# Kernel tuning notes

Hardware: AMD Instinct MI355X
Metric: run time of the kernel (lower is better)

## Reference

```python
import jax, jax.numpy as jnp
import numpy as np

V, E, H, B, P, Q = 100000, 300, 256, 64, 400, 50
NEG = -1e7


def _gru_param(k, s=0.08):
    k1, k2, k3, k4 = jax.random.split(k, 4)
    return (jax.random.normal(k1, (2, 3 * H, E)) * s,
            jax.random.normal(k2, (2, 3 * H, H)) * s,
            jax.random.normal(k3, (2, 3 * H)) * s,
            jax.random.normal(k4, (2, 3 * H)) * s)


def setup_inputs() -> dict:
    key = jax.random.key(0)
    ks = jax.random.split(key, 10)
    emb = (jax.random.normal(ks[0], (V, E)) * 0.1).at[0].set(0.0)  # padding_idx=0 row zeroed
    passage = jax.random.randint(ks[1], (B, P), 1, V)
    question = jax.random.randint(ks[2], (B, Q), 1, V)
    # variable lengths, padding (token 0) at the tail like pack_padded_sequence assumes
    p_len = 200 + (jnp.arange(B) * 7) % (P - 200)
    q_len = 20 + (jnp.arange(B) * 3) % (Q - 20)
    passage = jnp.where(jnp.arange(P)[None, :] < p_len[:, None], passage, 0)
    question = jnp.where(jnp.arange(Q)[None, :] < q_len[:, None], question, 0)
    pW_ih, pW_hh, pb_ih, pb_hh = _gru_param(ks[3])
    qW_ih, qW_hh, qb_ih, qb_hh = _gru_param(ks[4])
    start_w = jax.random.normal(ks[5], (6 * H,)) * 0.05
    start_b = jax.random.normal(ks[6], ()) * 0.05
    end_w = jax.random.normal(ks[7], (6 * H,)) * 0.05
    end_b = jax.random.normal(ks[8], ()) * 0.05
    return dict(passage=passage, question=question, emb=emb,
                pW_ih=pW_ih, pW_hh=pW_hh, pb_ih=pb_ih, pb_hh=pb_hh,
                qW_ih=qW_ih, qW_hh=qW_hh, qb_ih=qb_ih, qb_hh=qb_hh,
                start_w=start_w, start_b=start_b, end_w=end_w, end_b=end_b)


def bi_gru(x, mask, Wih, Whh, bih, bhh):
    """Bidirectional GRU with packed-sequence-equivalent masking.
    x: (B,T,E), mask: (B,T) float. Returns (B,T,2H). Padded outputs are 0,
    and the backward pass starts at the true last token (mask freezes state)."""
    m = mask[..., None]                                          # (B,T,1)
    xproj = jnp.einsum('bte,dhe->dbth', x, Wih) + bih[:, None, None, :]  # (2,B,T,3H)

    def run(xp, mm, Whh_d, bhh_d):
        def step(h, inp):
            xt, mt = inp                                         # (B,3H),(B,1)
            hp = h @ Whh_d.T + bhh_d
            r = jax.nn.sigmoid(xt[:, :H] + hp[:, :H])
            z = jax.nn.sigmoid(xt[:, H:2 * H] + hp[:, H:2 * H])
            n = jnp.tanh(xt[:, 2 * H:] + r * hp[:, 2 * H:])
            h_new = (1 - z) * n + z * h
            h_new = mt * h_new + (1 - mt) * h
            return h_new, h_new * mt
        h0 = jnp.zeros((xp.shape[0], H), xp.dtype)
        _, out = jax.lax.scan(step, h0, (xp.transpose(1, 0, 2), mm.transpose(1, 0, 2)))
        return out.transpose(1, 0, 2)                            # (B,T,H)

    fwd = run(xproj[0], m, Whh[0], bhh[0])
    bwd = run(xproj[1][:, ::-1], m[:, ::-1], Whh[1], bhh[1])[:, ::-1]
    return jnp.concatenate([fwd, bwd], axis=-1)


def reference(passage, question, emb,
              pW_ih, pW_hh, pb_ih, pb_hh,
              qW_ih, qW_hh, qb_ih, qb_hh,
              start_w, start_b, end_w, end_b):
    p_mask = (passage != 0).astype(jnp.float32)                  # (B,P)
    q_mask = (question != 0).astype(jnp.float32)                 # (B,Q)
    Hp = bi_gru(emb[passage], p_mask, pW_ih, pW_hh, pb_ih, pb_hh)  # (B,P,2H)
    Hq = bi_gru(emb[question], q_mask, qW_ih, qW_hh, qb_ih, qb_hh)  # (B,Q,2H)

    # Trilinear attention: decompose Linear over the cat([p, q, p*q]) terms
    w1, w2, w3 = start_w[:2 * H], start_w[2 * H:4 * H], start_w[4 * H:]
    scores = (Hp @ w1)[:, :, None] + (Hq @ w2)[:, None, :] \
        + jnp.einsum('bpd,bqd->bpq', Hp * w3, Hq) + start_b      # (B,P,Q)

    # allennlp masked_softmax: softmax(vector*mask) * mask, renormalized
    a = jax.nn.softmax(scores * q_mask[:, None, :], axis=-1) * q_mask[:, None, :]
    a = a / (a.sum(axis=-1, keepdims=True) + 1e-13)

    wavg = jnp.einsum('bpq,bqd->bpd', a, Hq)                     # (B,P,2H)
    combined = jnp.concatenate([Hp, wavg, Hp * wavg], axis=-1)   # (B,P,6H)

    start_logits = jnp.where(p_mask > 0, combined @ start_w + start_b, NEG)
    end_logits = jnp.where(p_mask > 0, combined @ end_w + end_b, NEG)
    log_mask = jnp.log(p_mask + 1e-45)
    softmax_start = jax.nn.log_softmax(start_logits + log_mask, axis=-1)
    softmax_end = jax.nn.log_softmax(end_logits + log_mask, axis=-1)
    return start_logits, end_logits, softmax_start, softmax_end
```

## Files before the change

kernel.cpp:

```cpp
#include <hip/hip_runtime.h>
#include <math.h>

constexpr int Bb = 64;
constexpr int Pp = 400;
constexpr int Qq = 50;
constexpr int Ee = 300;
constexpr int Hh = 256;
constexpr int H3 = 768;
constexpr int Dd = 512;

#define NEGC (-10000000.0f)
#define LOGTINY (-103.278929903f)

typedef _Float16 h2 __attribute__((ext_vector_type(2)));
typedef _Float16 f16x8 __attribute__((ext_vector_type(8)));
typedef float f32x4 __attribute__((ext_vector_type(4)));

__device__ __forceinline__ float allred(float v){
  #pragma unroll
  for (int off = 1; off < 64; off <<= 1) v += __shfl_xor(v, off);
  return v;
}
__device__ __forceinline__ float allmax(float v){
  #pragma unroll
  for (int off = 1; off < 64; off <<= 1) v = fmaxf(v, __shfl_xor(v, off));
  return v;
}
__device__ __forceinline__ float sigm(float x){ return 1.f / (1.f + expf(-x)); }

__device__ __forceinline__ float dot2f(unsigned a, unsigned b, float c){
#if __has_builtin(__builtin_amdgcn_fdot2)
  return __builtin_amdgcn_fdot2(__builtin_bit_cast(h2, a), __builtin_bit_cast(h2, b), c, false);
#else
  float r = c;
  asm("v_dot2_f32_f16 %0, %1, %2, %0" : "+v"(r) : "v"(a), "v"(b));
  return r;
#endif
}

#define U4C(v,c) ((c)==0?(v).x:((c)==1?(v).y:((c)==2?(v).z:(v).w)))

__global__ __launch_bounds__(256) void prep_emb16(const float* __restrict__ emb,
                                                  _Float16* __restrict__ emb16){
  size_t idx = (size_t)blockIdx.x * 256 + threadIdx.x;
  if (idx >= (size_t)100000 * 160) return;
  int col2 = (int)(idx % 160);
  size_t row = idx / 160;
  int c = col2 * 2;
  float2 v = make_float2(0.f, 0.f);
  if (c < Ee) v = *(const float2*)(emb + row * Ee + c);
  h2 o = { (_Float16)v.x, (_Float16)v.y };
  *(h2*)(emb16 + row * 320 + c) = o;
}

__global__ __launch_bounds__(256) void prep_wih16(const float* __restrict__ pW,
                                                  const float* __restrict__ qW,
                                                  _Float16* __restrict__ wih16){
  int idx = blockIdx.x * 256 + threadIdx.x;
  if (idx >= 2 * 2 * 768 * 160) return;
  int col2 = idx % 160;
  int r = idx / 160;
  int g = r / 1536;
  int dh = r % 1536;
  int c = col2 * 2;
  const float* W = g ? qW : pW;
  float2 v = make_float2(0.f, 0.f);
  if (c < Ee) v = *(const float2*)(W + (size_t)dh * Ee + c);
  h2 o = { (_Float16)v.x, (_Float16)v.y };
  *(h2*)(wih16 + (size_t)r * 320 + c) = o;
}

__global__ __launch_bounds__(256) void prep_w16(const float* __restrict__ pW,
                                                const float* __restrict__ qW,
                                                unsigned* __restrict__ w16){
  int idx = blockIdx.x * 256 + threadIdx.x;
  if (idx >= 2 * 2 * 3 * 16 * 512 * 4) return;
  int c = idx & 3;
  int t = (idx >> 2) & 511;
  int q = (idx >> 11) & 15;
  int gg = idx >> 15;
  int gate = gg % 3, gd = gg / 3;
  int d = gd & 1, g = gd >> 1;
  int j = t & 255, half = t >> 8;
  int p = half * 64 + q * 4 + c;
  int row = gate * 256 + j;
  const float* W = g ? qW : pW;
  const float* src = W + ((size_t)d * H3 + row) * Hh + 2 * p;
  _Float16 a = (_Float16)src[0], b = (_Float16)src[1];
  unsigned short ua, ub;
  __builtin_memcpy(&ua, &a, 2); __builtin_memcpy(&ub, &b, 2);
  unsigned val = (unsigned)ua | ((unsigned)ub << 16);

  size_t u4idx;
  if (q < 4)       u4idx = ((size_t)gg * 4 + q) * 512 + t;
  else if (q < 10) u4idx = 24576 + ((size_t)gg * 6 + (q - 4)) * 512 + t;
  else             u4idx = 61440 + ((size_t)gg * 6 + (q - 10)) * 512 + t;
  w16[u4idx * 4 + c] = val;
}

__global__ __launch_bounds__(512) void xproj_mfma(const int* __restrict__ tok,
                                                  const _Float16* __restrict__ emb16,
                                                  const _Float16* __restrict__ wih16,
                                                  const float* __restrict__ bih,
                                                  _Float16* __restrict__ xp, int T){
  __shared__ __align__(16) _Float16 Af[128][72];
  __shared__ __align__(16) _Float16 Bf[128][72];
  int tid = threadIdx.x;
  int m0 = blockIdx.y * 128;
  int nt = blockIdx.x;
  int d = nt / 6, h0 = (nt % 6) * 128;
  int wid = tid >> 6, lane = tid & 63;
  int wr = wid >> 2, wc = wid & 3;

  int r0 = tid >> 3;
  int r1 = (tid + 512) >> 3;
  int cc = (tid & 7) * 8;
  const _Float16* eA0 = emb16 + (size_t)tok[m0 + r0] * 320;
  const _Float16* eA1 = emb16 + (size_t)tok[m0 + r1] * 320;
  const _Float16* wB0 = wih16 + ((size_t)d * H3 + h0 + r0) * 320;
  const _Float16* wB1 = wih16 + ((size_t)d * H3 + h0 + r1) * 320;

  f32x4 acc[4][2] = {};

  for (int k0 = 0; k0 < 320; k0 += 64){
    *(f16x8*)&Af[r0][cc] = *(const f16x8*)(eA0 + k0 + cc);
    *(f16x8*)&Af[r1][cc] = *(const f16x8*)(eA1 + k0 + cc);
    *(f16x8*)&Bf[r0][cc] = *(const f16x8*)(wB0 + k0 + cc);
    *(f16x8*)&Bf[r1][cc] = *(const f16x8*)(wB1 + k0 + cc);
    __syncthreads();
    #pragma unroll
    for (int kc = 0; kc < 2; ++kc){
      int kb = kc * 32 + (lane >> 4) * 8;
      f16x8 af[4], bf[2];
      #pragma unroll
      for (int i = 0; i < 4; ++i) af[i] = *(const f16x8*)&Af[wr * 64 + i * 16 + (lane & 15)][kb];
      #pragma unroll
      for (int jn = 0; jn < 2; ++jn) bf[jn] = *(const f16x8*)&Bf[wc * 32 + jn * 16 + (lane & 15)][kb];
      #pragma unroll
      for (int i = 0; i < 4; ++i)
        #pragma unroll
        for (int jn = 0; jn < 2; ++jn)
          acc[i][jn] = __builtin_amdgcn_mfma_f32_16x16x32_f16(af[i], bf[jn], acc[i][jn], 0, 0, 0);
    }
    __syncthreads();
  }

  #pragma unroll
  for (int jn = 0; jn < 2; ++jn){
    int h = h0 + wc * 32 + jn * 16 + (lane & 15);
    float bv = bih[d * H3 + h];
    #pragma unroll
    for (int i = 0; i < 4; ++i){
      #pragma unroll
      for (int r = 0; r < 4; ++r){
        int m = m0 + wr * 64 + i * 16 + (lane >> 4) * 4 + r;
        int bI = m / T, tI = m - bI * T;
        xp[(((size_t)d * Bb + bI) * T + tI) * H3 + h] = (_Float16)(acc[i][jn][r] + bv);
      }
    }
  }
}

__global__ __launch_bounds__(512)
void gru_kernel(const int* __restrict__ ptok,
                const int* __restrict__ qtok,
                const _Float16* __restrict__ xpp,
                const _Float16* __restrict__ xpq,
                const unsigned* __restrict__ w16,
                const float* __restrict__ pbhh,
                const float* __restrict__ qbhh,
                float* __restrict__ Hp,
                float* __restrict__ Hq){
  int wg = blockIdx.x;
  bool isp = wg < 128;
  int lw = isp ? wg : wg - 128;
  int d = lw & 1, b = lw >> 1;
  int T = isp ? Pp : Qq;
  const int* tok = (isp ? ptok : qtok) + b * T;
  const _Float16* xrow = (isp ? xpp : xpq) + ((size_t)d * Bb + b) * T * H3;
  int gd = (isp ? 0 : 2) + d;
  const float* bhh = (isp ? pbhh : qbhh) + d * H3;
  float* Hout = (isp ? Hp : Hq) + (size_t)b * T * Dd + d * Hh;

  __shared__ __align__(16) uint4 ldsW[18 * 512];
  __shared__ unsigned hbuf[2][128];
  __shared__ float pa[Hh], pb[Hh], pn[Hh];

  int t = threadIdx.x;
  int j = t & 255, half = t >> 8, lane = t & 63;

  const uint4* wR = (const uint4*)w16 + (size_t)(gd * 3) * 4 * 512;
  unsigned wr0[16], wr1[16], wr2[16];
  #pragma unroll
  for (int q = 0; q < 4; ++q){
    uint4 v0 = wR[(0 * 4 + q) * 512 + t];
    uint4 v1 = wR[(1 * 4 + q) * 512 + t];
    uint4 v2 = wR[(2 * 4 + q) * 512 + t];
    wr0[4 * q + 0] = v0.x; wr0[4 * q + 1] = v0.y; wr0[4 * q + 2] = v0.z; wr0[4 * q + 3] = v0.w;
    wr1[4 * q + 0] = v1.x; wr1[4 * q + 1] = v1.y; wr1[4 * q + 2] = v1.z; wr1[4 * q + 3] = v1.w;
    wr2[4 * q + 0] = v2.x; wr2[4 * q + 1] = v2.y; wr2[4 * q + 2] = v2.z; wr2[4 * q + 3] = v2.w;
  }
  #pragma unroll
  for (int i = 0; i < 16; ++i){
    asm volatile("" : "+v"(wr0[i]));
    asm volatile("" : "+v"(wr1[i]));
    asm volatile("" : "+v"(wr2[i]));
  }
  const uint4* wL = (const uint4*)w16 + 24576 + (size_t)(gd * 3) * 6 * 512;
  #pragma unroll
  for (int u = 0; u < 18; ++u) ldsW[u * 512 + t] = wL[u * 512 + t];
  const uint4* wS = (const uint4*)w16 + 61440 + (size_t)(gd * 3) * 6 * 512;

  float bh0 = bhh[j], bh1 = bhh[Hh + j], bh2 = bhh[2 * Hh + j];
  float h_old = 0.f;
  if (t < 128) hbuf[1][t] = 0u;
  __syncthreads();

  int t0 = d ? (T - 1) : 0;
  float pre0 = 0.f, pre1 = 0.f, pre2 = 0.f;
  if (half == 0){
    pre0 = (float)xrow[(size_t)t0 * H3 + j];
    pre1 = (float)xrow[(size_t)t0 * H3 + Hh + j];
    pre2 = (float)xrow[(size_t)t0 * H3 + 2 * Hh + j];
  }

  for (int s = 0; s < T; ++s){
    int tt = d ? (T - 1 - s) : s;
    unsigned vh = hbuf[(s + 1) & 1][half * 64 + lane];
    float a0 = 0.f, a1 = 0.f, a2 = 0.f;

    uint4 sA0 = wS[0 * 512 + t], sA1 = wS[1 * 512 + t], sA2 = wS[2 * 512 + t],
          sA3 = wS[3 * 512 + t], sA4 = wS[4 * 512 + t], sA5 = wS[5 * 512 + t];
    uint4 sB0 = wS[6 * 512 + t],  sB1 = wS[7 * 512 + t],  sB2 = wS[8 * 512 + t],
          sB3 = wS[9 * 512 + t],  sB4 = wS[10 * 512 + t], sB5 = wS[11 * 512 + t];

    #pragma unroll
    for (int q = 0; q < 4; ++q)
      #pragma unroll
      for (int c = 0; c < 4; ++c){
        unsigned hv = (unsigned)__builtin_amdgcn_readlane((int)vh, q * 4 + c);
        a0 = dot2f(wr0[4 * q + c], hv, a0);
        a1 = dot2f(wr1[4 * q + c], hv, a1);
        a2 = dot2f(wr2[4 * q + c], hv, a2);
      }

    uint4 sC0 = wS[12 * 512 + t], sC1 = wS[13 * 512 + t], sC2 = wS[14 * 512 + t],
          sC3 = wS[15 * 512 + t], sC4 = wS[16 * 512 + t], sC5 = wS[17 * 512 + t];

    #pragma unroll
    for (int qb = 0; qb < 6; ++qb){
      uint4 l0 = ldsW[(0 * 6 + qb) * 512 + t];
      uint4 l1 = ldsW[(1 * 6 + qb) * 512 + t];
      uint4 l2 = ldsW[(2 * 6 + qb) * 512 + t];
      #pragma unroll
      for (int c = 0; c < 4; ++c){
        unsigned hv = (unsigned)__builtin_amdgcn_readlane((int)vh, 16 + qb * 4 + c);
        a0 = dot2f(U4C(l0, c), hv, a0);
        a1 = dot2f(U4C(l1, c), hv, a1);
        a2 = dot2f(U4C(l2, c), hv, a2);
      }
    }

    #define CONS(v, qi, ACC) { _Pragma("unroll") \
      for (int c = 0; c < 4; ++c){ \
        unsigned hv = (unsigned)__builtin_amdgcn_readlane((int)vh, 40 + (qi) * 4 + c); \
        ACC = dot2f(U4C(v, c), hv, ACC); } }
    CONS(sA0, 0, a0) CONS(sA1, 1, a0) CONS(sA2, 2, a0)
    CONS(sA3, 3, a0) CONS(sA4, 4, a0) CONS(sA5, 5, a0)
    CONS(sB0, 0, a1) CONS(sB1, 1, a1) CONS(sB2, 2, a1)
    CONS(sB3, 3, a1) CONS(sB4, 4, a1) CONS(sB5, 5, a1)
    CONS(sC0, 0, a2) CONS(sC1, 1, a2) CONS(sC2, 2, a2)
    CONS(sC3, 3, a2) CONS(sC4, 4, a2) CONS(sC5, 5, a2)
    #undef CONS

    if (half == 1){ pa[j] = a0; pb[j] = a1; pn[j] = a2; }
    __syncthreads();
    if (half == 0){
      float xt0 = pre0, xt1 = pre1, xt2 = pre2;
      if (s + 1 < T){
        int tn = d ? (T - 2 - s) : (s + 1);
        pre0 = (float)xrow[(size_t)tn * H3 + j];
        pre1 = (float)xrow[(size_t)tn * H3 + Hh + j];
        pre2 = (float)xrow[(size_t)tn * H3 + 2 * Hh + j];
      }
      float g0 = a0 + pa[j] + bh0;
      float g1 = a1 + pb[j] + bh1;
      float g2 = a2 + pn[j] + bh2;
      float r = sigm(xt0 + g0);
      float z = sigm(xt1 + g1);
      float n = tanhf(xt2 + r * g2);
      float hnew = (1.f - z) * n + z * h_old;
      float m = (tok[tt] != 0) ? 1.f : 0.f;
      float hm = m * hnew + (1.f - m) * h_old;
      h_old = hm;
      ((_Float16*)hbuf[s & 1])[j] = (_Float16)hm;
      Hout[(size_t)tt * Dd + j] = hm * m;
    }
    __syncthreads();
  }
}

__global__ __launch_bounds__(512) void attn_kernel(const float* __restrict__ Hp,
                                                   const float* __restrict__ Hq,
                                                   const int* __restrict__ ptok,
                                                   const int* __restrict__ qtok,
                                                   const float* __restrict__ start_w,
                                                   const float* __restrict__ sbp,
                                                   const float* __restrict__ end_w,
                                                   const float* __restrict__ ebp,
                                                   float* __restrict__ out){
  extern __shared__ __align__(16) float lds[];
  float* hqs = lds;
  float* s2s = hqs + Qq * Dd;
  float* qms = s2s + 64;
  float* scw = qms + 64;
  float* aw  = scw + 512;

  int b = blockIdx.y, pc = blockIdx.x;
  int tid = threadIdx.x, wid = tid >> 6, lane = tid & 63;
  float sb = sbp[0], eb = ebp[0];

  float w1r[8], w2r[8], w3r[8], e1r[8], e2r[8], e3r[8];
  #pragma unroll
  for (int i = 0; i < 8; ++i){
    int c = lane * 8 + i;
    w1r[i] = start_w[c]; w2r[i] = start_w[Dd + c]; w3r[i] = start_w[2 * Dd + c];
    e1r[i] = end_w[c];   e2r[i] = end_w[Dd + c];   e3r[i] = end_w[2 * Dd + c];
  }
  for (int idx = tid; idx < Qq * Dd; idx += 512) hqs[idx] = Hq[(size_t)b * Qq * Dd + idx];
  __syncthreads();

  for (int q = wid; q < Qq; q += 8){
    float part = 0.f;
    const float* hq = hqs + q * Dd + lane * 8;
    #pragma unroll
    for (int i = 0; i < 8; ++i) part += hq[i] * w2r[i];
    part = allred(part);
    if (lane == 0){
      s2s[q] = part;
      qms[q] = (qtok[b * Qq + q] != 0) ? 1.f : 0.f;
    }
  }
  __syncthreads();

  for (int p = pc * 100 + wid; p < pc * 100 + 100; p += 8){
    const float* hprow = Hp + ((size_t)b * Pp + p) * Dd + lane * 8;
    float4 hv0 = *(const float4*)hprow;
    float4 hv1 = *(const float4*)(hprow + 4);
    float hpc[8] = {hv0.x, hv0.y, hv0.z, hv0.w, hv1.x, hv1.y, hv1.z, hv1.w};
    float hw3[8], he3[8];
    float s1 = 0.f, ed = 0.f;
    #pragma unroll
    for (int i = 0; i < 8; ++i){
      hw3[i] = hpc[i] * w3r[i];
      he3[i] = hpc[i] * e3r[i];
      s1 += hpc[i] * w1r[i];
      ed += hpc[i] * e1r[i];
    }
    #pragma unroll
    for (int off = 1; off < 64; off <<= 1){
      s1 += __shfl_xor(s1, off);
      ed += __shfl_xor(ed, off);
    }
    for (int q = 0; q < Qq; ++q){
      const float4* hq4 = (const float4*)(hqs + q * Dd + lane * 8);
      float4 a0 = hq4[0], a1 = hq4[1];
      float dot = hw3[0] * a0.x + hw3[1] * a0.y + hw3[2] * a0.z + hw3[3] * a0.w
                + hw3[4] * a1.x + hw3[5] * a1.y + hw3[6] * a1.z + hw3[7] * a1.w;
      dot = allred(dot);
      if (lane == 0) scw[wid * 64 + q] = (s1 + s2s[q] + dot + sb) * qms[q];
    }
    float v = (lane < Qq) ? scw[wid * 64 + lane] : -1e30f;
    float M = allmax(v);
    float ev = (lane < Qq) ? expf(v - M) : 0.f;
    float S = allred(ev);
    float am = (lane < Qq) ? (ev / S) * qms[lane] : 0.f;
    float Sm = allred(am);
    float af = am / (Sm + 1e-13f);
    if (lane < Qq) aw[wid * 64 + lane] = af;
    float wv[8] = {0.f, 0.f, 0.f, 0.f, 0.f, 0.f, 0.f, 0.f};
    for (int q = 0; q < Qq; ++q){
      float aq = aw[wid * 64 + q];
      const float4* hq4 = (const float4*)(hqs + q * Dd + lane * 8);
      float4 a0 = hq4[0], a1 = hq4[1];
      wv[0] += aq * a0.x; wv[1] += aq * a0.y; wv[2] += aq * a0.z; wv[3] += aq * a0.w;
      wv[4] += aq * a1.x; wv[5] += aq * a1.y; wv[6] += aq * a1.z; wv[7] += aq * a1.w;
    }
    float acc2 = 0.f, acc3 = 0.f, acc4 = 0.f, acc5 = 0.f;
    #pragma unroll
    for (int i = 0; i < 8; ++i){
      acc2 += wv[i] * w2r[i];
      acc3 += hw3[i] * wv[i];
      acc4 += wv[i] * e2r[i];
      acc5 += he3[i] * wv[i];
    }
    #pragma unroll
    for (int off = 1; off < 64; off <<= 1){
      acc2 += __shfl_xor(acc2, off);
      acc3 += __shfl_xor(acc3, off);
      acc4 += __shfl_xor(acc4, off);
      acc5 += __shfl_xor(acc5, off);
    }
    if (lane == 0){
      bool pm = (ptok[b * Pp + p] != 0);
      out[(size_t)b * Pp + p]                   = pm ? (s1 + acc2 + acc3 + sb) : NEGC;
      out[(size_t)Bb * Pp + (size_t)b * Pp + p] = pm ? (ed + acc4 + acc5 + eb) : NEGC;
    }
  }
}

__global__ __launch_bounds__(512) void lsm_kernel(const int* __restrict__ ptok,
                                                  float* __restrict__ out){
  int b = blockIdx.x >> 1, sel = blockIdx.x & 1;
  const float* lg = out + (size_t)sel * Bb * Pp + (size_t)b * Pp;
  float* o = out + (size_t)(2 + sel) * Bb * Pp + (size_t)b * Pp;
  int tid = threadIdx.x;
  __shared__ float red1[8];
  __shared__ float red2[8];
  float x = -1e30f;
  if (tid < Pp) x = lg[tid] + ((ptok[b * Pp + tid] != 0) ? 0.f : LOGTINY);
  float m = allmax(x);
  if ((tid & 63) == 0) red1[tid >> 6] = m;
  __syncthreads();
  float M = red1[0];
  #pragma unroll
  for (int i = 1; i < 8; ++i) M = fmaxf(M, red1[i]);
  float e = (tid < Pp) ? expf(x - M) : 0.f;
  float s = allred(e);
  if ((tid & 63) == 0) red2[tid >> 6] = s;
  __syncthreads();
  float S = 0.f;
  #pragma unroll
  for (int i = 0; i < 8; ++i) S += red2[i];
  if (tid < Pp) o[tid] = (x - M) - logf(S);
}

extern "C" void kernel_launch(void* const* d_in, const int* in_sizes, int n_in,
                              void* d_out, int out_size, void* d_ws, size_t ws_size,
                              hipStream_t stream){
  const int*   passage  = (const int*)d_in[0];
  const int*   question = (const int*)d_in[1];
  const float* emb      = (const float*)d_in[2];
  const float* pW_ih    = (const float*)d_in[3];
  const float* pW_hh    = (const float*)d_in[4];
  const float* pb_ih    = (const float*)d_in[5];
  const float* pb_hh    = (const float*)d_in[6];
  const float* qW_ih    = (const float*)d_in[7];
  const float* qW_hh    = (const float*)d_in[8];
  const float* qb_ih    = (const float*)d_in[9];
  const float* qb_hh    = (const float*)d_in[10];
  const float* start_w  = (const float*)d_in[11];
  const float* start_b  = (const float*)d_in[12];
  const float* end_w    = (const float*)d_in[13];
  const float* end_b    = (const float*)d_in[14];
  float* out = (float*)d_out;

  float*     ws    = (float*)d_ws;
  unsigned*  w16   = (unsigned*)ws;
  _Float16*  emb16 = (_Float16*)(ws + 393216);
  _Float16*  wih16 = (_Float16*)(ws + 16393216);
  _Float16*  xpp   = (_Float16*)(ws + 16884736);
  _Float16*  xpq   = (_Float16*)(ws + 36545536);
  float*     Hp    = ws + 39003136;
  float*     Hq    = ws + 52110336;

  hipLaunchKernelGGL(prep_w16, dim3(1536), dim3(256), 0, stream, pW_hh, qW_hh, w16);
  hipLaunchKernelGGL(prep_emb16, dim3(62500), dim3(256), 0, stream, emb, emb16);
  hipLaunchKernelGGL(prep_wih16, dim3(1920), dim3(256), 0, stream, pW_ih, qW_ih, wih16);
  hipLaunchKernelGGL(xproj_mfma, dim3(12, 200), dim3(512), 0, stream,
                     passage, emb16, wih16, pb_ih, xpp, Pp);
  hipLaunchKernelGGL(xproj_mfma, dim3(12, 25), dim3(512), 0, stream,
                     question, emb16, wih16 + (size_t)2 * H3 * 320, qb_ih, xpq, Qq);
  hipLaunchKernelGGL(gru_kernel, dim3(256), dim3(512), 0, stream,
                     passage, question, xpp, xpq, w16, pb_hh, qb_hh, Hp, Hq);
  size_t attn_lds = (size_t)(Qq * Dd + 64 + 64 + 512 + 512) * sizeof(float);
  hipLaunchKernelGGL(attn_kernel, dim3(4, 64), dim3(512), attn_lds, stream,
                     Hp, Hq, passage, question, start_w, start_b, end_w, end_b, out);
  hipLaunchKernelGGL(lsm_kernel, dim3(128), dim3(512), 0, stream, passage, out);
}
```

Baseline: 964.3 us.

## Run GRU recurrence with one thread per hidden unit, dropping split-K reduction

The GRU recurrent kernel now uses 256 threads per block, each owning a full 256-long dot product for its hidden unit, instead of 512 threads splitting the K dimension in two. This removes the LDS partial-sum exchange and one barrier per timestep. The weight split is rebalanced: 120 packed registers hold 40 columns, LDS holds 48, and 40 stream from global memory in an interleaved order, with prep_w16 rewritten to the new layout. In exchange each thread does twice the dot work per step and carries heavy register pressure, which risks spills.

Measured after the change: 1.752 ms. 1.82x slower.

```diff
diff --git a/kernel.cpp b/kernel.cpp
--- a/kernel.cpp
+++ b/kernel.cpp
@@ -74,28 +74,24 @@
                                                 const float* __restrict__ qW,
                                                 unsigned* __restrict__ w16){
   int idx = blockIdx.x * 256 + threadIdx.x;
-  if (idx >= 2 * 2 * 3 * 16 * 512 * 4) return;
+  if (idx >= 4 * 96 * 256 * 4) return;
   int c = idx & 3;
-  int t = (idx >> 2) & 511;
-  int q = (idx >> 11) & 15;
-  int gg = idx >> 15;
-  int gate = gg % 3, gd = gg / 3;
-  int d = gd & 1, g = gd >> 1;
-  int j = t & 255, half = t >> 8;
-  int p = half * 64 + q * 4 + c;
-  int row = gate * 256 + j;
-  const float* W = g ? qW : pW;
+  int j = (idx >> 2) & 255;
+  int rest = idx >> 10;
+  int b = rest % 96;
+  int gd = rest / 96;
+  int d = gd & 1, kind = gd >> 1;
+  int g, p;
+  if (b < 30){ g = b / 10; p = 4 * (b % 10) + c; }
+  else if (b < 66){ int v = b - 30; g = v / 12; p = 40 + 4 * (v % 12) + c; }
+  else { int v = b - 66; int i = v / 3; g = v % 3; p = 88 + 4 * i + c; }
+  int row = g * 256 + j;
+  const float* W = kind ? qW : pW;
   const float* src = W + ((size_t)d * H3 + row) * Hh + 2 * p;
-  _Float16 a = (_Float16)src[0], b = (_Float16)src[1];
+  _Float16 a = (_Float16)src[0], bb = (_Float16)src[1];
   unsigned short ua, ub;
-  __builtin_memcpy(&ua, &a, 2); __builtin_memcpy(&ub, &b, 2);
-  unsigned val = (unsigned)ua | ((unsigned)ub << 16);
-
-  size_t u4idx;
-  if (q < 4)       u4idx = ((size_t)gg * 4 + q) * 512 + t;
-  else if (q < 10) u4idx = 24576 + ((size_t)gg * 6 + (q - 4)) * 512 + t;
-  else             u4idx = 61440 + ((size_t)gg * 6 + (q - 10)) * 512 + t;
-  w16[u4idx * 4 + c] = val;
+  __builtin_memcpy(&ua, &a, 2); __builtin_memcpy(&ub, &bb, 2);
+  w16[idx] = (unsigned)ua | ((unsigned)ub << 16);
 }
 
 __global__ __launch_bounds__(512) void xproj_mfma(const int* __restrict__ tok,
@@ -161,7 +157,7 @@
   }
 }
 
-__global__ __launch_bounds__(512)
+__global__ __launch_bounds__(256, 1)
 void gru_kernel(const int* __restrict__ ptok,
                 const int* __restrict__ qtok,
                 const _Float16* __restrict__ xpp,
@@ -182,120 +178,120 @@
   const float* bhh = (isp ? pbhh : qbhh) + d * H3;
   float* Hout = (isp ? Hp : Hq) + (size_t)b * T * Dd + d * Hh;
 
-  __shared__ __align__(16) uint4 ldsW[18 * 512];
+  __shared__ __align__(16) uint4 ldsW[36 * 256];
   __shared__ unsigned hbuf[2][128];
-  __shared__ float pa[Hh], pb[Hh], pn[Hh];
-
-  int t = threadIdx.x;
-  int j = t & 255, half = t >> 8, lane = t & 63;
-
-  const uint4* wR = (const uint4*)w16 + (size_t)(gd * 3) * 4 * 512;
-  unsigned wr0[16], wr1[16], wr2[16];
-  #pragma unroll
-  for (int q = 0; q < 4; ++q){
-    uint4 v0 = wR[(0 * 4 + q) * 512 + t];
-    uint4 v1 = wR[(1 * 4 + q) * 512 + t];
-    uint4 v2 = wR[(2 * 4 + q) * 512 + t];
-    wr0[4 * q + 0] = v0.x; wr0[4 * q + 1] = v0.y; wr0[4 * q + 2] = v0.z; wr0[4 * q + 3] = v0.w;
-    wr1[4 * q + 0] = v1.x; wr1[4 * q + 1] = v1.y; wr1[4 * q + 2] = v1.z; wr1[4 * q + 3] = v1.w;
-    wr2[4 * q + 0] = v2.x; wr2[4 * q + 1] = v2.y; wr2[4 * q + 2] = v2.z; wr2[4 * q + 3] = v2.w;
-  }
-  #pragma unroll
-  for (int i = 0; i < 16; ++i){
-    asm volatile("" : "+v"(wr0[i]));
-    asm volatile("" : "+v"(wr1[i]));
-    asm volatile("" : "+v"(wr2[i]));
-  }
-  const uint4* wL = (const uint4*)w16 + 24576 + (size_t)(gd * 3) * 6 * 512;
-  #pragma unroll
-  for (int u = 0; u < 18; ++u) ldsW[u * 512 + t] = wL[u * 512 + t];
-  const uint4* wS = (const uint4*)w16 + 61440 + (size_t)(gd * 3) * 6 * 512;
+
+  int j = threadIdx.x, lane = j & 63;
+  const uint4* wq = (const uint4*)w16 + (size_t)gd * 96 * 256;
+
+  unsigned wr[120];
+  #pragma unroll
+  for (int bq = 0; bq < 30; ++bq){
+    uint4 v = wq[bq * 256 + j];
+    wr[4 * bq + 0] = v.x; wr[4 * bq + 1] = v.y; wr[4 * bq + 2] = v.z; wr[4 * bq + 3] = v.w;
+  }
+  #pragma unroll
+  for (int i = 0; i < 120; ++i) asm volatile("" : "+v"(wr[i]));
+
+  #pragma unroll
+  for (int bq = 0; bq < 36; ++bq) ldsW[bq * 256 + j] = wq[(30 + bq) * 256 + j];
+  const uint4* wS = wq + 66 * 256;
 
   float bh0 = bhh[j], bh1 = bhh[Hh + j], bh2 = bhh[2 * Hh + j];
   float h_old = 0.f;
-  if (t < 128) hbuf[1][t] = 0u;
+  if (j < 128) hbuf[1][j] = 0u;
   __syncthreads();
 
   int t0 = d ? (T - 1) : 0;
-  float pre0 = 0.f, pre1 = 0.f, pre2 = 0.f;
-  if (half == 0){
-    pre0 = (float)xrow[(size_t)t0 * H3 + j];
-    pre1 = (float)xrow[(size_t)t0 * H3 + Hh + j];
-    pre2 = (float)xrow[(size_t)t0 * H3 + 2 * Hh + j];
-  }
+  float pre0 = (float)xrow[(size_t)t0 * H3 + j];
+  float pre1 = (float)xrow[(size_t)t0 * H3 + Hh + j];
+  float pre2 = (float)xrow[(size_t)t0 * H3 + 2 * Hh + j];
 
   for (int s = 0; s < T; ++s){
     int tt = d ? (T - 1 - s) : s;
-    unsigned vh = hbuf[(s + 1) & 1][half * 64 + lane];
+    const unsigned* hb = hbuf[(s + 1) & 1];
+    unsigned vh0 = hb[lane];
+    unsigned vh1 = hb[64 + lane];
     float a0 = 0.f, a1 = 0.f, a2 = 0.f;
 
-    uint4 sA0 = wS[0 * 512 + t], sA1 = wS[1 * 512 + t], sA2 = wS[2 * 512 + t],
-          sA3 = wS[3 * 512 + t], sA4 = wS[4 * 512 + t], sA5 = wS[5 * 512 + t];
-    uint4 sB0 = wS[6 * 512 + t],  sB1 = wS[7 * 512 + t],  sB2 = wS[8 * 512 + t],
-          sB3 = wS[9 * 512 + t],  sB4 = wS[10 * 512 + t], sB5 = wS[11 * 512 + t];
-
-    #pragma unroll
-    for (int q = 0; q < 4; ++q)
+    #define LPH(q) { \
+      uint4 l0 = ldsW[(q) * 256 + j]; \
+      uint4 l1 = ldsW[(12 + (q)) * 256 + j]; \
+      uint4 l2 = ldsW[(24 + (q)) * 256 + j]; \
+      _Pragma("unroll") \
+      for (int c = 0; c < 4; ++c){ \
+        int p = 40 + 4 * (q) + c; \
+        unsigned hv = (unsigned)__builtin_amdgcn_readlane((int)(p < 64 ? vh0 : vh1), p & 63); \
+        a0 = dot2f(U4C(l0, c), hv, a0); \
+        a1 = dot2f(U4C(l1, c), hv, a1); \
+        a2 = dot2f(U4C(l2, c), hv, a2); } }
+    #define SCON(i, A, B, C) { \
+      _Pragma("unroll") \
+      for (int c = 0; c < 4; ++c){ \
+        unsigned hv = (unsigned)__builtin_amdgcn_readlane((int)vh1, 24 + 4 * (i) + c); \
+        a0 = dot2f(U4C(A, c), hv, a0); \
+        a1 = dot2f(U4C(B, c), hv, a1); \
+        a2 = dot2f(U4C(C, c), hv, a2); } }
+    #define SISS(i, A, B, C) \
+      uint4 A = wS[((i) * 3 + 0) * 256 + j]; \
+      uint4 B = wS[((i) * 3 + 1) * 256 + j]; \
+      uint4 C = wS[((i) * 3 + 2) * 256 + j];
+
+    SISS(0, g0a, g0b, g0c)
+    SISS(1, g1a, g1b, g1c)
+
+    #pragma unroll
+    for (int q = 0; q < 10; ++q)
       #pragma unroll
       for (int c = 0; c < 4; ++c){
-        unsigned hv = (unsigned)__builtin_amdgcn_readlane((int)vh, q * 4 + c);
-        a0 = dot2f(wr0[4 * q + c], hv, a0);
-        a1 = dot2f(wr1[4 * q + c], hv, a1);
-        a2 = dot2f(wr2[4 * q + c], hv, a2);
+        unsigned hv = (unsigned)__builtin_amdgcn_readlane((int)vh0, 4 * q + c);
+        a0 = dot2f(wr[q * 4 + c], hv, a0);
+        a1 = dot2f(wr[40 + q * 4 + c], hv, a1);
+        a2 = dot2f(wr[80 + q * 4 + c], hv, a2);
       }
 
-    uint4 sC0 = wS[12 * 512 + t], sC1 = wS[13 * 512 + t], sC2 = wS[14 * 512 + t],
-          sC3 = wS[15 * 512 + t], sC4 = wS[16 * 512 + t], sC5 = wS[17 * 512 + t];
-
-    #pragma unroll
-    for (int qb = 0; qb < 6; ++qb){
-      uint4 l0 = ldsW[(0 * 6 + qb) * 512 + t];
-      uint4 l1 = ldsW[(1 * 6 + qb) * 512 + t];
-      uint4 l2 = ldsW[(2 * 6 + qb) * 512 + t];
-      #pragma unroll
-      for (int c = 0; c < 4; ++c){
-        unsigned hv = (unsigned)__builtin_amdgcn_readlane((int)vh, 16 + qb * 4 + c);
-        a0 = dot2f(U4C(l0, c), hv, a0);
-        a1 = dot2f(U4C(l1, c), hv, a1);
-        a2 = dot2f(U4C(l2, c), hv, a2);
-      }
-    }
-
-    #define CONS(v, qi, ACC) { _Pragma("unroll") \
-      for (int c = 0; c < 4; ++c){ \
-        unsigned hv = (unsigned)__builtin_amdgcn_readlane((int)vh, 40 + (qi) * 4 + c); \
-        ACC = dot2f(U4C(v, c), hv, ACC); } }
-    CONS(sA0, 0, a0) CONS(sA1, 1, a0) CONS(sA2, 2, a0)
-    CONS(sA3, 3, a0) CONS(sA4, 4, a0) CONS(sA5, 5, a0)
-    CONS(sB0, 0, a1) CONS(sB1, 1, a1) CONS(sB2, 2, a1)
-    CONS(sB3, 3, a1) CONS(sB4, 4, a1) CONS(sB5, 5, a1)
-    CONS(sC0, 0, a2) CONS(sC1, 1, a2) CONS(sC2, 2, a2)
-    CONS(sC3, 3, a2) CONS(sC4, 4, a2) CONS(sC5, 5, a2)
-    #undef CONS
-
-    if (half == 1){ pa[j] = a0; pb[j] = a1; pn[j] = a2; }
-    __syncthreads();
-    if (half == 0){
-      float xt0 = pre0, xt1 = pre1, xt2 = pre2;
-      if (s + 1 < T){
-        int tn = d ? (T - 2 - s) : (s + 1);
-        pre0 = (float)xrow[(size_t)tn * H3 + j];
-        pre1 = (float)xrow[(size_t)tn * H3 + Hh + j];
-        pre2 = (float)xrow[(size_t)tn * H3 + 2 * Hh + j];
-      }
-      float g0 = a0 + pa[j] + bh0;
-      float g1 = a1 + pb[j] + bh1;
-      float g2 = a2 + pn[j] + bh2;
-      float r = sigm(xt0 + g0);
-      float z = sigm(xt1 + g1);
-      float n = tanhf(xt2 + r * g2);
-      float hnew = (1.f - z) * n + z * h_old;
-      float m = (tok[tt] != 0) ? 1.f : 0.f;
-      float hm = m * hnew + (1.f - m) * h_old;
-      h_old = hm;
-      ((_Float16*)hbuf[s & 1])[j] = (_Float16)hm;
-      Hout[(size_t)tt * Dd + j] = hm * m;
-    }
+    SISS(2, g2a, g2b, g2c)
+    SISS(3, g3a, g3b, g3c)
+    LPH(0) LPH(1) LPH(2)
+    SCON(0, g0a, g0b, g0c)
+    SISS(4, g4a, g4b, g4c)
+    SISS(5, g5a, g5b, g5c)
+    LPH(3) LPH(4) LPH(5)
+    SCON(1, g1a, g1b, g1c)
+    SISS(6, g6a, g6b, g6c)
+    SISS(7, g7a, g7b, g7c)
+    LPH(6) LPH(7) LPH(8)
+    SCON(2, g2a, g2b, g2c)
+    SISS(8, g8a, g8b, g8c)
+    SISS(9, g9a, g9b, g9c)
+    LPH(9) LPH(10) LPH(11)
+    SCON(3, g3a, g3b, g3c)
+    SCON(4, g4a, g4b, g4c)
+    SCON(5, g5a, g5b, g5c)
+    SCON(6, g6a, g6b, g6c)
+    SCON(7, g7a, g7b, g7c)
+    SCON(8, g8a, g8b, g8c)
+    SCON(9, g9a, g9b, g9c)
+    #undef LPH
+    #undef SCON
+    #undef SISS
+
+    float xt0 = pre0, xt1 = pre1, xt2 = pre2;
+    if (s + 1 < T){
+      int tn = d ? (T - 2 - s) : (s + 1);
+      pre0 = (float)xrow[(size_t)tn * H3 + j];
+      pre1 = (float)xrow[(size_t)tn * H3 + Hh + j];
+      pre2 = (float)xrow[(size_t)tn * H3 + 2 * Hh + j];
+    }
+    float r = sigm(xt0 + a0 + bh0);
+    float z = sigm(xt1 + a1 + bh1);
+    float n = tanhf(xt2 + r * (a2 + bh2));
+    float hnew = (1.f - z) * n + z * h_old;
+    float m = (tok[tt] != 0) ? 1.f : 0.f;
+    float hm = m * hnew + (1.f - m) * h_old;
+    h_old = hm;
+    ((_Float16*)hbuf[s & 1])[j] = (_Float16)hm;
+    Hout[(size_t)tt * Dd + j] = hm * m;
     __syncthreads();
   }
 }
@@ -471,7 +467,7 @@
                      passage, emb16, wih16, pb_ih, xpp, Pp);
   hipLaunchKernelGGL(xproj_mfma, dim3(12, 25), dim3(512), 0, stream,
                      question, emb16, wih16 + (size_t)2 * H3 * 320, qb_ih, xpq, Qq);
-  hipLaunchKernelGGL(gru_kernel, dim3(256), dim3(512), 0, stream,
+  hipLaunchKernelGGL(gru_kernel, dim3(256), dim3(256), 0, stream,
                      passage, question, xpp, xpq, w16, pb_hh, qb_hh, Hp, Hq);
   size_t attn_lds = (size_t)(Qq * Dd + 64 + 64 + 512 + 512) * sizeof(float);
   hipLaunchKernelGGL(attn_kernel, dim3(4, 64), dim3(512), attn_lds, stream,
```

## Batch GRU recurrence over 16 sequences per workgroup using MFMA matmuls

Applied to the files above, without the earlier changes.

Before, each workgroup ran one sequence and direction, computing the recurrent matvec with dot2 instructions and weights split across registers, LDS and global reloads. Now each workgroup handles 16 batch rows of one direction and GRU. The whole W_hh (fp16) is held in registers in MFMA B-fragment layout, and each step does a 16x256x768 mfma_f32_16x16x32_f16 product from a shared hidden-state tile. This cuts the grid from 256 to 16 workgroups, trading parallelism and CU occupancy for far less weight traffic per step. It also replaces tanhf with a clamped exp-based tanh.

New measurement: 2.354 ms. 2.44x slower.

```diff
diff --git a/kernel.cpp b/kernel.cpp
--- a/kernel.cpp
+++ b/kernel.cpp
@@ -27,18 +27,11 @@
   return v;
 }
 __device__ __forceinline__ float sigm(float x){ return 1.f / (1.f + expf(-x)); }
-
-__device__ __forceinline__ float dot2f(unsigned a, unsigned b, float c){
-#if __has_builtin(__builtin_amdgcn_fdot2)
-  return __builtin_amdgcn_fdot2(__builtin_bit_cast(h2, a), __builtin_bit_cast(h2, b), c, false);
-#else
-  float r = c;
-  asm("v_dot2_f32_f16 %0, %1, %2, %0" : "+v"(r) : "v"(a), "v"(b));
-  return r;
-#endif
-}
-
-#define U4C(v,c) ((c)==0?(v).x:((c)==1?(v).y:((c)==2?(v).z:(v).w)))
+__device__ __forceinline__ float tanh_c(float x){
+  x = fminf(fmaxf(x, -15.f), 15.f);
+  float e = expf(2.f * x);
+  return (e - 1.f) / (e + 1.f);
+}
 
 __global__ __launch_bounds__(256) void prep_emb16(const float* __restrict__ emb,
                                                   _Float16* __restrict__ emb16){
@@ -70,32 +63,26 @@
   *(h2*)(wih16 + (size_t)r * 320 + c) = o;
 }
 
-__global__ __launch_bounds__(256) void prep_w16(const float* __restrict__ pW,
-                                                const float* __restrict__ qW,
-                                                unsigned* __restrict__ w16){
+__global__ __launch_bounds__(256) void prep_wB(const float* __restrict__ pW,
+                                               const float* __restrict__ qW,
+                                               uint4* __restrict__ wB){
   int idx = blockIdx.x * 256 + threadIdx.x;
-  if (idx >= 2 * 2 * 3 * 16 * 512 * 4) return;
-  int c = idx & 3;
-  int t = (idx >> 2) & 511;
-  int q = (idx >> 11) & 15;
-  int gg = idx >> 15;
-  int gate = gg % 3, gd = gg / 3;
-  int d = gd & 1, g = gd >> 1;
-  int j = t & 255, half = t >> 8;
-  int p = half * 64 + q * 4 + c;
-  int row = gate * 256 + j;
-  const float* W = g ? qW : pW;
-  const float* src = W + ((size_t)d * H3 + row) * Hh + 2 * p;
-  _Float16 a = (_Float16)src[0], b = (_Float16)src[1];
-  unsigned short ua, ub;
-  __builtin_memcpy(&ua, &a, 2); __builtin_memcpy(&ub, &b, 2);
-  unsigned val = (unsigned)ua | ((unsigned)ub << 16);
-
-  size_t u4idx;
-  if (q < 4)       u4idx = ((size_t)gg * 4 + q) * 512 + t;
-  else if (q < 10) u4idx = 24576 + ((size_t)gg * 6 + (q - 4)) * 512 + t;
-  else             u4idx = 61440 + ((size_t)gg * 6 + (q - 10)) * 512 + t;
-  w16[u4idx * 4 + c] = val;
+  if (idx >= 98304) return;
+  int lane = idx & 63;
+  int r = idx >> 6;
+  int cp = r % 6; r /= 6;
+  int kt = r % 8; r /= 8;
+  int w  = r % 8; r /= 8;
+  int gd = r;
+  int d = gd & 1, kind = gd >> 1;
+  int g = cp >> 1, cg = cp & 1;
+  int n  = g * 256 + w * 32 + cg * 16 + (lane & 15);
+  int k0 = kt * 32 + (lane >> 4) * 8;
+  const float* W = kind ? qW : pW;
+  const float* src = W + ((size_t)d * H3 + n) * Hh + k0;
+  f16x8 v = { (_Float16)src[0], (_Float16)src[1], (_Float16)src[2], (_Float16)src[3],
+              (_Float16)src[4], (_Float16)src[5], (_Float16)src[6], (_Float16)src[7] };
+  wB[idx] = __builtin_bit_cast(uint4, v);
 }
 
 __global__ __launch_bounds__(512) void xproj_mfma(const int* __restrict__ tok,
@@ -166,135 +153,83 @@
                 const int* __restrict__ qtok,
                 const _Float16* __restrict__ xpp,
                 const _Float16* __restrict__ xpq,
-                const unsigned* __restrict__ w16,
+                const uint4* __restrict__ wB,
                 const float* __restrict__ pbhh,
                 const float* __restrict__ qbhh,
                 float* __restrict__ Hp,
                 float* __restrict__ Hq){
-  int wg = blockIdx.x;
-  bool isp = wg < 128;
-  int lw = isp ? wg : wg - 128;
-  int d = lw & 1, b = lw >> 1;
+  int wgid = blockIdx.x;
+  int gd = wgid >> 2, bg = wgid & 3;
+  bool isp = gd < 2;
+  int d = gd & 1;
   int T = isp ? Pp : Qq;
-  const int* tok = (isp ? ptok : qtok) + b * T;
-  const _Float16* xrow = (isp ? xpp : xpq) + ((size_t)d * Bb + b) * T * H3;
-  int gd = (isp ? 0 : 2) + d;
+  const int* tok = isp ? ptok : qtok;
+  const _Float16* xbase = (isp ? xpp : xpq) + (size_t)d * Bb * T * H3;
   const float* bhh = (isp ? pbhh : qbhh) + d * H3;
-  float* Hout = (isp ? Hp : Hq) + (size_t)b * T * Dd + d * Hh;
-
-  __shared__ __align__(16) uint4 ldsW[18 * 512];
-  __shared__ unsigned hbuf[2][128];
-  __shared__ float pa[Hh], pb[Hh], pn[Hh];
-
-  int t = threadIdx.x;
-  int j = t & 255, half = t >> 8, lane = t & 63;
-
-  const uint4* wR = (const uint4*)w16 + (size_t)(gd * 3) * 4 * 512;
-  unsigned wr0[16], wr1[16], wr2[16];
-  #pragma unroll
-  for (int q = 0; q < 4; ++q){
-    uint4 v0 = wR[(0 * 4 + q) * 512 + t];
-    uint4 v1 = wR[(1 * 4 + q) * 512 + t];
-    uint4 v2 = wR[(2 * 4 + q) * 512 + t];
-    wr0[4 * q + 0] = v0.x; wr0[4 * q + 1] = v0.y; wr0[4 * q + 2] = v0.z; wr0[4 * q + 3] = v0.w;
-    wr1[4 * q + 0] = v1.x; wr1[4 * q + 1] = v1.y; wr1[4 * q + 2] = v1.z; wr1[4 * q + 3] = v1.w;
-    wr2[4 * q + 0] = v2.x; wr2[4 * q + 1] = v2.y; wr2[4 * q + 2] = v2.z; wr2[4 * q + 3] = v2.w;
-  }
-  #pragma unroll
-  for (int i = 0; i < 16; ++i){
-    asm volatile("" : "+v"(wr0[i]));
-    asm volatile("" : "+v"(wr1[i]));
-    asm volatile("" : "+v"(wr2[i]));
-  }
-  const uint4* wL = (const uint4*)w16 + 24576 + (size_t)(gd * 3) * 6 * 512;
-  #pragma unroll
-  for (int u = 0; u < 18; ++u) ldsW[u * 512 + t] = wL[u * 512 + t];
-  const uint4* wS = (const uint4*)w16 + 61440 + (size_t)(gd * 3) * 6 * 512;
-
-  float bh0 = bhh[j], bh1 = bhh[Hh + j], bh2 = bhh[2 * Hh + j];
-  float h_old = 0.f;
-  if (t < 128) hbuf[1][t] = 0u;
+  float* Hbase = isp ? Hp : Hq;
+
+  __shared__ _Float16 hbuf[2][16][264];
+
+  int t = threadIdx.x, wv = t >> 6, lane = t & 63;
+
+  f16x8 B[8][6];
+  const uint4* wb = wB + ((size_t)(gd * 8 + wv)) * 48 * 64;
+  #pragma unroll
+  for (int kt = 0; kt < 8; ++kt)
+    #pragma unroll
+    for (int cp = 0; cp < 6; ++cp)
+      B[kt][cp] = __builtin_bit_cast(f16x8, wb[(kt * 6 + cp) * 64 + lane]);
+
+  int j0 = wv * 32 + (lane & 15);
+  float bias[3][2];
+  #pragma unroll
+  for (int g = 0; g < 3; ++g){
+    bias[g][0] = bhh[g * 256 + j0];
+    bias[g][1] = bhh[g * 256 + j0 + 16];
+  }
+
+  float hold[2][4] = {};
+  for (int i = t; i < 16 * 264; i += 512) ((_Float16*)hbuf[1])[i] = (_Float16)0.f;
   __syncthreads();
-
-  int t0 = d ? (T - 1) : 0;
-  float pre0 = 0.f, pre1 = 0.f, pre2 = 0.f;
-  if (half == 0){
-    pre0 = (float)xrow[(size_t)t0 * H3 + j];
-    pre1 = (float)xrow[(size_t)t0 * H3 + Hh + j];
-    pre2 = (float)xrow[(size_t)t0 * H3 + 2 * Hh + j];
-  }
 
   for (int s = 0; s < T; ++s){
     int tt = d ? (T - 1 - s) : s;
-    unsigned vh = hbuf[(s + 1) & 1][half * 64 + lane];
-    float a0 = 0.f, a1 = 0.f, a2 = 0.f;
-
-    uint4 sA0 = wS[0 * 512 + t], sA1 = wS[1 * 512 + t], sA2 = wS[2 * 512 + t],
-          sA3 = wS[3 * 512 + t], sA4 = wS[4 * 512 + t], sA5 = wS[5 * 512 + t];
-    uint4 sB0 = wS[6 * 512 + t],  sB1 = wS[7 * 512 + t],  sB2 = wS[8 * 512 + t],
-          sB3 = wS[9 * 512 + t],  sB4 = wS[10 * 512 + t], sB5 = wS[11 * 512 + t];
-
-    #pragma unroll
-    for (int q = 0; q < 4; ++q)
-      #pragma unroll
-      for (int c = 0; c < 4; ++c){
-        unsigned hv = (unsigned)__builtin_amdgcn_readlane((int)vh, q * 4 + c);
-        a0 = dot2f(wr0[4 * q + c], hv, a0);
-        a1 = dot2f(wr1[4 * q + c], hv, a1);
-        a2 = dot2f(wr2[4 * q + c], hv, a2);
+    const _Float16* hp = &hbuf[(s + 1) & 1][lane & 15][(lane >> 4) * 8];
+
+    f32x4 acc[6] = {};
+    #pragma unroll
+    for (int kt = 0; kt < 8; ++kt){
+      f16x8 aF = *(const f16x8*)(hp + kt * 32);
+      #pragma unroll
+      for (int cp = 0; cp < 6; ++cp)
+        acc[cp] = __builtin_amdgcn_mfma_f32_16x16x32_f16(aF, B[kt][cp], acc[cp], 0, 0, 0);
+    }
+
+    #pragma unroll
+    for (int r = 0; r < 4; ++r){
+      int bl = (lane >> 4) * 4 + r;
+      int b = bg * 16 + bl;
+      float m = (tok[b * T + tt] != 0) ? 1.f : 0.f;
+      const _Float16* xr = xbase + ((size_t)b * T + tt) * H3;
+      float* ho = Hbase + ((size_t)b * T + tt) * Dd + d * Hh;
+      #pragma unroll
+      for (int cg = 0; cg < 2; ++cg){
+        int j = j0 + cg * 16;
+        float pr = acc[0 * 2 + cg][r] + bias[0][cg];
+        float pz = acc[1 * 2 + cg][r] + bias[1][cg];
+        float pn = acc[2 * 2 + cg][r] + bias[2][cg];
+        float x0 = (float)xr[j];
+        float x1 = (float)xr[256 + j];
+        float x2 = (float)xr[512 + j];
+        float rg = sigm(x0 + pr);
+        float zg = sigm(x1 + pz);
+        float ng = tanh_c(x2 + rg * pn);
+        float hv = (1.f - zg) * ng + zg * hold[cg][r];
+        float hm = m * hv + (1.f - m) * hold[cg][r];
+        hold[cg][r] = hm;
+        hbuf[s & 1][bl][j] = (_Float16)hm;
+        ho[j] = hm * m;
       }
-
-    uint4 sC0 = wS[12 * 512 + t], sC1 = wS[13 * 512 + t], sC2 = wS[14 * 512 + t],
-          sC3 = wS[15 * 512 + t], sC4 = wS[16 * 512 + t], sC5 = wS[17 * 512 + t];
-
-    #pragma unroll
-    for (int qb = 0; qb < 6; ++qb){
-      uint4 l0 = ldsW[(0 * 6 + qb) * 512 + t];
-      uint4 l1 = ldsW[(1 * 6 + qb) * 512 + t];
-      uint4 l2 = ldsW[(2 * 6 + qb) * 512 + t];
-      #pragma unroll
-      for (int c = 0; c < 4; ++c){
-        unsigned hv = (unsigned)__builtin_amdgcn_readlane((int)vh, 16 + qb * 4 + c);
-        a0 = dot2f(U4C(l0, c), hv, a0);
-        a1 = dot2f(U4C(l1, c), hv, a1);
-        a2 = dot2f(U4C(l2, c), hv, a2);
-      }
-    }
-
-    #define CONS(v, qi, ACC) { _Pragma("unroll") \
-      for (int c = 0; c < 4; ++c){ \
-        unsigned hv = (unsigned)__builtin_amdgcn_readlane((int)vh, 40 + (qi) * 4 + c); \
-        ACC = dot2f(U4C(v, c), hv, ACC); } }
-    CONS(sA0, 0, a0) CONS(sA1, 1, a0) CONS(sA2, 2, a0)
-    CONS(sA3, 3, a0) CONS(sA4, 4, a0) CONS(sA5, 5, a0)
-    CONS(sB0, 0, a1) CONS(sB1, 1, a1) CONS(sB2, 2, a1)
-    CONS(sB3, 3, a1) CONS(sB4, 4, a1) CONS(sB5, 5, a1)
-    CONS(sC0, 0, a2) CONS(sC1, 1, a2) CONS(sC2, 2, a2)
-    CONS(sC3, 3, a2) CONS(sC4, 4, a2) CONS(sC5, 5, a2)
-    #undef CONS
-
-    if (half == 1){ pa[j] = a0; pb[j] = a1; pn[j] = a2; }
-    __syncthreads();
-    if (half == 0){
-      float xt0 = pre0, xt1 = pre1, xt2 = pre2;
-      if (s + 1 < T){
-        int tn = d ? (T - 2 - s) : (s + 1);
-        pre0 = (float)xrow[(size_t)tn * H3 + j];
-        pre1 = (float)xrow[(size_t)tn * H3 + Hh + j];
-        pre2 = (float)xrow[(size_t)tn * H3 + 2 * Hh + j];
-      }
-      float g0 = a0 + pa[j] + bh0;
-      float g1 = a1 + pb[j] + bh1;
-      float g2 = a2 + pn[j] + bh2;
-      float r = sigm(xt0 + g0);
-      float z = sigm(xt1 + g1);
-      float n = tanhf(xt2 + r * g2);
-      float hnew = (1.f - z) * n + z * h_old;
-      float m = (tok[tt] != 0) ? 1.f : 0.f;
-      float hm = m * hnew + (1.f - m) * h_old;
-      h_old = hm;
-      ((_Float16*)hbuf[s & 1])[j] = (_Float16)hm;
-      Hout[(size_t)tt * Dd + j] = hm * m;
     }
     __syncthreads();
   }
@@ -456,7 +391,7 @@
   float* out = (float*)d_out;
 
   float*     ws    = (float*)d_ws;
-  unsigned*  w16   = (unsigned*)ws;
+  uint4*     wB    = (uint4*)ws;
   _Float16*  emb16 = (_Float16*)(ws + 393216);
   _Float16*  wih16 = (_Float16*)(ws + 16393216);
   _Float16*  xpp   = (_Float16*)(ws + 16884736);
@@ -464,15 +399,15 @@
   float*     Hp    = ws + 39003136;
   float*     Hq    = ws + 52110336;
 
-  hipLaunchKernelGGL(prep_w16, dim3(1536), dim3(256), 0, stream, pW_hh, qW_hh, w16);
+  hipLaunchKernelGGL(prep_wB, dim3(384), dim3(256), 0, stream, pW_hh, qW_hh, wB);
   hipLaunchKernelGGL(prep_emb16, dim3(62500), dim3(256), 0, stream, emb, emb16);
   hipLaunchKernelGGL(prep_wih16, dim3(1920), dim3(256), 0, stream, pW_ih, qW_ih, wih16);
   hipLaunchKernelGGL(xproj_mfma, dim3(12, 200), dim3(512), 0, stream,
                      passage, emb16, wih16, pb_ih, xpp, Pp);
   hipLaunchKernelGGL(xproj_mfma, dim3(12, 25), dim3(512), 0, stream,
                      question, emb16, wih16 + (size_t)2 * H3 * 320, qb_ih, xpq, Qq);
-  hipLaunchKernelGGL(gru_kernel, dim3(256), dim3(512), 0, stream,
-                     passage, question, xpp, xpq, w16, pb_hh, qb_hh, Hp, Hq);
+  hipLaunchKernelGGL(gru_kernel, dim3(16), dim3(512), 0, stream,
+                     passage, question, xpp, xpq, wB, pb_hh, qb_hh, Hp, Hq);
   size_t attn_lds = (size_t)(Qq * Dd + 64 + 64 + 512 + 512) * sizeof(float);
   hipLaunchKernelGGL(attn_kernel, dim3(4, 64), dim3(512), attn_lds, stream,
                      Hp, Hq, passage, question, start_w, start_b, end_w, end_b, out);
```
